# Optimization experiments

Measured on AMD Instinct MI355X. Metric: run time of the kernel, lower is better.

Reference implementation:

```python
import jax, jax.numpy as jnp
import numpy as np

K = 20
BN_EPS = 1e-5


def setup_inputs() -> dict:
    key = jax.random.key(0)
    ks = jax.random.split(key, 6)
    B, N, H = 2, 4096, 384
    s = lambda k, sh, sc: jax.random.normal(k, sh, dtype=jnp.float32) * sc
    return {
        "xyz": jax.random.normal(ks[0], (B, N, 3), dtype=jnp.float32),
        "W1": s(ks[1], (6, 128), 0.2),   "b1": jnp.zeros((128,), jnp.float32),
        "g1": jnp.ones((128,), jnp.float32), "be1": jnp.zeros((128,), jnp.float32),
        "W2": s(ks[2], (128, 256), 0.08), "b2": jnp.zeros((256,), jnp.float32),
        "W3": s(ks[3], (512, 512), 0.05), "b3": jnp.zeros((512,), jnp.float32),
        "g3": jnp.ones((512,), jnp.float32), "be3": jnp.zeros((512,), jnp.float32),
        "W4": s(ks[4], (512, H), 0.05),  "b4": jnp.zeros((H,), jnp.float32),
    }


def _knn_idx(x, k):
    # x: [B,N,3] -> k nearest neighbor indices (incl. self), sorted by distance
    sq = jnp.sum(x * x, axis=-1)                                  # [B,N]
    d2 = sq[:, :, None] + sq[:, None, :] - 2.0 * jnp.einsum('bnd,bmd->bnm', x, x)
    _, idx = jax.lax.top_k(-d2, k)                                # [B,N,k]
    return jax.lax.stop_gradient(idx)


def _bn_relu(h, gamma, beta):
    # BatchNorm1d in training mode: per-channel stats over (batch, length) dims.
    # h: [M, k, C]
    mu = jnp.mean(h, axis=(0, 1), keepdims=True)
    var = jnp.var(h, axis=(0, 1), keepdims=True)  # biased, matches torch BN
    return jax.nn.relu((h - mu) * jax.lax.rsqrt(var + BN_EPS) * gamma + beta)


def reference(xyz, W1, b1, g1, be1, W2, b2, W3, b3, g3, be3, W4, b4):
    B, N, _ = xyz.shape
    idx = _knn_idx(xyz, K)                                        # [B,N,K]
    nbr = jax.vmap(lambda pts, i: pts[i])(xyz, idx)               # [B,N,K,3]
    ctr = xyz[:, :, None, :]
    edge = jnp.concatenate([nbr - ctr, jnp.broadcast_to(ctr, nbr.shape)], axis=-1)
    h = edge.reshape(B * N, K, 6)                                 # [M,K,6]
    # conv1: Conv1d(6,128) -> BN -> ReLU -> Conv1d(128,256)  (kernel-1 convs == matmul)
    h = _bn_relu(h @ W1 + b1, g1, be1)
    h = h @ W2 + b2                                               # [M,K,256]
    gmax = jnp.max(h, axis=1, keepdims=True)                      # [M,1,256]
    f = jnp.concatenate([jnp.broadcast_to(gmax, h.shape), h], axis=-1)  # [M,K,512]
    # conv2: Conv1d(512,512) -> BN -> ReLU -> Conv1d(512,hidden)
    f = _bn_relu(f @ W3 + b3, g3, be3)
    f = f @ W4 + b4                                               # [M,K,H]
    feature = jnp.max(f, axis=1).reshape(B, N, -1)                # [B,N,H]
    return (xyz, feature)
```

## Files before the change

### kernel.cpp

```cpp
#include <hip/hip_runtime.h>
#include <float.h>

#define NPTS_B 4096
#define NPTS 8192
#define KNN 20
#define NSAMP (NPTS*KNN)

typedef __attribute__((ext_vector_type(8))) short bf16x8;
typedef __attribute__((ext_vector_type(4))) float f32x4;

static __device__ __forceinline__ float bf2f(unsigned short u) {
  return __uint_as_float(((unsigned int)u) << 16);
}
static __device__ __forceinline__ unsigned short f2bf(float f) {
  unsigned int u = __float_as_uint(f);
  u += 0x7fffu + ((u >> 16) & 1u);
  return (unsigned short)(u >> 16);
}
static __device__ __forceinline__ void gl_lds16(const void* g, void* l) {
  __builtin_amdgcn_global_load_lds(
      (const __attribute__((address_space(1))) unsigned int*)g,
      (__attribute__((address_space(3))) unsigned int*)l, 16, 0, 0);
}

__global__ __launch_bounds__(256) void wprep_kernel(const float* __restrict__ W3,
                                                    const float* __restrict__ W4,
                                                    const float* __restrict__ W2,
                                                    unsigned short* __restrict__ W3T,
                                                    unsigned short* __restrict__ W4T,
                                                    unsigned short* __restrict__ W2T) {
  int id = blockIdx.x * 256 + threadIdx.x;
  if (id < 512*512) {
    int n = id >> 9, k = id & 511;
    W3T[id] = f2bf(W3[k*512 + n]);
  } else if (id < 512*512 + 384*512) {
    int id2 = id - 512*512;
    int n = id2 >> 9, k = id2 & 511;
    W4T[id2] = f2bf(W4[k*384 + n]);
  } else {
    int id2 = id - (512*512 + 384*512);
    int n = id2 >> 7, k = id2 & 127;
    W2T[id2] = f2bf(W2[k*256 + n]);
  }
}

__global__ __launch_bounds__(256) void xyzprep_kernel(const float* __restrict__ xyz,
                                                      float* __restrict__ xT) {
#pragma clang fp contract(off)
  int j = blockIdx.x * 256 + threadIdx.x;
  int b = j >> 12, jj = j & 4095;
  float x = xyz[j*3+0], y = xyz[j*3+1], z = xyz[j*3+2];
  float sq = (x*x + y*y) + z*z;
  float* base = xT + (size_t)b*16384;
  base[jj] = x; base[4096+jj] = y; base[8192+jj] = z; base[12288+jj] = sq;
}

__global__ __launch_bounds__(256) void knn_kernel(const float* __restrict__ xyz,
                                                  const float* __restrict__ xT,
                                                  int* __restrict__ idx,
                                                  float* __restrict__ out_xyz) {
#pragma clang fp contract(off)
  int p = blockIdx.x;
  int b = p >> 12;
  int base = b << 12;
  int tid = threadIdx.x;
  const float* xb = xT + (size_t)b*16384;
  float xi0 = xyz[p*3+0], xi1 = xyz[p*3+1], xi2 = xyz[p*3+2];
  float sqi = (xi0*xi0 + xi1*xi1) + xi2*xi2;

  __shared__ __align__(16) int hist[4096];
  __shared__ int sL1[256];
  __shared__ int nsel, binB;

#pragma unroll
  for (int u = 0; u < 16; ++u) hist[tid + (u << 8)] = 0;
  if (tid == 0) nsel = 0;
  __syncthreads();

  unsigned long long cand[16];
#pragma unroll
  for (int u = 0; u < 16; ++u) {
    int j = tid + (u << 8);
    float a0 = xb[j], a1 = xb[4096 + j], a2 = xb[8192 + j];
    float sqj = xb[12288 + j];
    float dt  = (xi0*a0 + xi1*a1) + xi2*a2;
    float d2  = (sqi + sqj) - 2.0f*dt;
    unsigned int kb = __float_as_uint(d2);
    cand[u] = ((unsigned long long)kb << 32) | (unsigned int)j;
    atomicAdd(&hist[kb >> 20], 1);
  }
  __syncthreads();

  {
    int s = 0;
#pragma unroll
    for (int u = 0; u < 16; ++u) s += hist[tid*16 + u];
    sL1[tid] = s;
  }
  __syncthreads();

  if (tid < 64) {
    int v = sL1[tid*4] + sL1[tid*4+1] + sL1[tid*4+2] + sL1[tid*4+3];
    int incl = v;
#pragma unroll
    for (int off = 1; off < 64; off <<= 1) {
      int t = __shfl_up(incl, off);
      if (tid >= off) incl += t;
    }
    unsigned long long ball = __ballot(incl >= KNN);
    int L = __ffsll(ball) - 1;
    if (tid == L) {
      int cum = incl - v;
      int bfound = -1;
      for (int t2 = 4*L; t2 < 4*L + 4; ++t2) {
        int s = sL1[t2];
        if (bfound < 0) {
          if (cum + s >= KNN) {
            for (int u = 0; u < 16; ++u) {
              int c = hist[t2*16 + u];
              if (cum + c >= KNN) { bfound = t2*16 + u; break; }
              cum += c;
            }
          } else {
            cum += s;
          }
        }
      }
      binB = bfound;
    }
  }
  __syncthreads();

  int B = binB;
  unsigned long long* list = (unsigned long long*)hist;
#pragma unroll
  for (int u = 0; u < 16; ++u) {
    if ((int)(unsigned int)(cand[u] >> 52) <= B) {
      int pos = atomicAdd(&nsel, 1);
      if (pos < 2048) list[pos] = cand[u];
    }
  }
  __syncthreads();

  int n = nsel; if (n > 2048) n = 2048;
  for (int t = tid; t < n; t += 256) {
    unsigned long long me = list[t];
    int rank = 0;
    for (int i = 0; i < n; ++i) rank += (list[i] < me);
    if (rank < KNN) idx[p*20 + rank] = base + (int)(me & 0xffffffffu);
  }
  if (tid < 3) out_xyz[p*3 + tid] = xyz[p*3 + tid];
}

__global__ __launch_bounds__(256) void h1_moments_kernel(const float* __restrict__ xyz,
                                                         const int* __restrict__ idx,
                                                         float* __restrict__ mbuck) {
  int tid = threadIdx.x, blk = blockIdx.x;
  float A[33] = {};
#pragma unroll
  for (int u = 0; u < 2; ++u) {
    int s = blk*512 + (u << 8) + tid;
    unsigned int p = (unsigned int)s / 20u;
    int jg = idx[s];
    float c0 = xyz[p*3+0], c1 = xyz[p*3+1], c2 = xyz[p*3+2];
    float e[6];
    e[0] = xyz[jg*3+0] - c0; e[1] = xyz[jg*3+1] - c1; e[2] = xyz[jg*3+2] - c2;
    e[3] = c0; e[4] = c1; e[5] = c2;
    int k = 6;
#pragma unroll
    for (int d = 0; d < 6; ++d) {
      A[d] += e[d];
#pragma unroll
      for (int d2 = d; d2 < 6; ++d2) { A[k] = fmaf(e[d], e[d2], A[k]); ++k; }
    }
  }
#pragma unroll
  for (int off = 1; off < 64; off <<= 1) {
#pragma unroll
    for (int i = 0; i < 33; ++i) A[i] += __shfl_xor(A[i], off);
  }
  if ((tid & 63) == 0) {
    int b = ((blk << 2) | (tid >> 6)) & 15;
    for (int i = 0; i < 33; ++i) atomicAdd(&mbuck[b*64 + i], A[i]);
  }
}

__global__ void bn_prep1(const float* __restrict__ W1, const float* __restrict__ b1,
                         const float* __restrict__ g1, const float* __restrict__ be1,
                         const float* __restrict__ mbuck, float* __restrict__ misc) {
  __shared__ float red[33];
  int tid = threadIdx.x;
  if (tid < 33) {
    float s = 0.f;
    for (int b = 0; b < 16; ++b) s += mbuck[b*64 + tid];
    red[tid] = s;
  }
  __syncthreads();
  int c = tid;
  float w[6];
#pragma unroll
  for (int d = 0; d < 6; ++d) w[d] = W1[d*128 + c];
  const float inv = 1.0f / (float)NSAMP;
  float t = 0.f;
#pragma unroll
  for (int d = 0; d < 6; ++d) t = fmaf(w[d], red[d], t);
  t *= inv;
  float Q = 0.f;
  int k = 6;
#pragma unroll
  for (int d = 0; d < 6; ++d) {
#pragma unroll
    for (int d2 = d; d2 < 6; ++d2) {
      float coef = (d == d2) ? w[d]*w[d] : 2.f*w[d]*w[d2];
      Q = fmaf(coef, red[k], Q); ++k;
    }
  }
  Q *= inv;
  float var = Q - t*t;
  float mu = b1[c] + t;
  float a = g1[c] / sqrtf(var + 1e-5f);
  misc[c] = a;
  misc[128 + c] = be1[c] - mu*a;
}

__global__ __launch_bounds__(256) void h2_kernel(const float* __restrict__ xyz,
                                                 const int* __restrict__ idx,
                                                 const float* __restrict__ W1,
                                                 const float* __restrict__ b1,
                                                 const unsigned short* __restrict__ W2T,
                                                 const float* __restrict__ b2,
                                                 const float* __restrict__ misc,
                                                 unsigned short* __restrict__ h2out,
                                                 unsigned short* __restrict__ gmaxout) {
  int p0 = blockIdx.x << 2;
  int tid = threadIdx.x;
  int w = tid >> 6, lane = tid & 63;
  int lr = lane & 15, lg = lane >> 4;
  __shared__ float e[80][6];
  __shared__ __align__(16) unsigned short As[80][136];
  __shared__ float pool[20][264];

  bf16x8 bfr[4][4];
#pragma unroll
  for (int j = 0; j < 4; ++j)
#pragma unroll
    for (int kk = 0; kk < 4; ++kk)
      bfr[j][kk] = *(const bf16x8*)(W2T + (size_t)(w*64 + j*16 + lr)*128 + kk*32 + lg*8);

  if (tid < 80) {
    int pl = (unsigned int)tid / 20u;
    int p = p0 + pl;
    int jg = idx[p0*20 + tid];
    float xi0 = xyz[p*3+0], xi1 = xyz[p*3+1], xi2 = xyz[p*3+2];
    e[tid][0] = xyz[jg*3+0] - xi0;
    e[tid][1] = xyz[jg*3+1] - xi1;
    e[tid][2] = xyz[jg*3+2] - xi2;
    e[tid][3] = xi0; e[tid][4] = xi1; e[tid][5] = xi2;
  }
  __syncthreads();

  {
    int c = tid & 127, half = tid >> 7;
    float w1v[6];
#pragma unroll
    for (int d = 0; d < 6; ++d) w1v[d] = W1[d*128 + c];
    float b1v = b1[c], a1 = misc[c], d1 = misc[128 + c];
#pragma unroll
    for (int u = 0; u < 40; ++u) {
      int row = (u << 1) | half;
      float v = b1v;
#pragma unroll
      for (int d = 0; d < 6; ++d) v = fmaf(e[row][d], w1v[d], v);
      v = fmaxf(fmaf(a1, v, d1), 0.f);
      As[row][c] = f2bf(v);
    }
  }
  __syncthreads();

  f32x4 acc[5][4] = {};
#pragma unroll
  for (int kk = 0; kk < 4; ++kk) {
    bf16x8 a[5];
#pragma unroll
    for (int i = 0; i < 5; ++i)
      a[i] = *(const bf16x8*)&As[i*16 + lr][kk*32 + lg*8];
#pragma unroll
    for (int i = 0; i < 5; ++i)
#pragma unroll
      for (int j = 0; j < 4; ++j)
        acc[i][j] = __builtin_amdgcn_mfma_f32_16x16x32_bf16(a[i], bfr[j][kk], acc[i][j], 0, 0, 0);
  }

  float b2v[4];
#pragma unroll
  for (int j = 0; j < 4; ++j) b2v[j] = b2[w*64 + j*16 + lr];
#pragma unroll
  for (int i = 0; i < 5; ++i) {
    int rbase = p0*20 + i*16 + lg*4;
#pragma unroll
    for (int j = 0; j < 4; ++j) {
      int col = w*64 + j*16 + lr;
      float v0 = acc[i][j][0] + b2v[j];
      float v1 = acc[i][j][1] + b2v[j];
      float v2 = acc[i][j][2] + b2v[j];
      float v3 = acc[i][j][3] + b2v[j];
      h2out[(size_t)(rbase+0)*256 + col] = f2bf(v0);
      h2out[(size_t)(rbase+1)*256 + col] = f2bf(v1);
      h2out[(size_t)(rbase+2)*256 + col] = f2bf(v2);
      h2out[(size_t)(rbase+3)*256 + col] = f2bf(v3);
      pool[i*4 + lg][col] = fmaxf(fmaxf(v0, v1), fmaxf(v2, v3));
    }
  }
  __syncthreads();
#pragma unroll
  for (int l = 0; l < 4; ++l) {
    int id = tid + (l << 8);
    int q = id >> 8, col = id & 255;
    float v = pool[q*5][col];
#pragma unroll
    for (int u = 1; u < 5; ++u) v = fmaxf(v, pool[q*5 + u][col]);
    gmaxout[(size_t)(p0 + q)*256 + col] = f2bf(v);
  }
}

__global__ __launch_bounds__(256) void pgemm_kernel(const unsigned short* __restrict__ gmax,
                                                    const unsigned short* __restrict__ W3T,
                                                    unsigned short* __restrict__ Pg) {
  int bid = blockIdx.x;
  int bm = bid >> 1, bn = bid & 1;
  int m0 = bm << 6, n0 = bn << 8;
  int tid = threadIdx.x;
  int lane = tid & 63, w = tid >> 6;
  int lr = lane & 15, lg = lane >> 4;
  __shared__ __align__(16) char smem[40960];
  unsigned short (*As)[64] = (unsigned short (*)[64])smem;
  unsigned short (*Bs)[64] = (unsigned short (*)[64])(smem + 8192);
  unsigned short (*Cs)[264] = (unsigned short (*)[264])smem;

  int swz = lr >> 1;
  f32x4 acc[4][4] = {};
  for (int kc = 0; kc < 256; kc += 64) {
#pragma unroll
    for (int l = 0; l < 2; ++l) {
      int id = tid + (l << 8);
      int row = id >> 3, ks = id & 7, kg = ks ^ ((id >> 4) & 7);
      gl_lds16(gmax + (size_t)(m0 + row)*256 + kc + (kg << 3), &As[row][ks << 3]);
    }
#pragma unroll
    for (int l = 0; l < 8; ++l) {
      int id = tid + (l << 8);
      int row = id >> 3, ks = id & 7, kg = ks ^ ((id >> 4) & 7);
      gl_lds16(W3T + (size_t)(n0 + row)*512 + kc + (kg << 3), &Bs[row][ks << 3]);
    }
    __syncthreads();
#pragma unroll
    for (int h = 0; h < 2; ++h) {
      int ch = ((h << 2) | lg) ^ swz;
      bf16x8 a[4], b[4];
#pragma unroll
      for (int t = 0; t < 4; ++t)
        a[t] = *(const bf16x8*)&As[t*16 + lr][ch << 3];
#pragma unroll
      for (int t = 0; t < 4; ++t)
        b[t] = *(const bf16x8*)&Bs[w*64 + t*16 + lr][ch << 3];
#pragma unroll
      for (int i = 0; i < 4; ++i)
#pragma unroll
        for (int j = 0; j < 4; ++j)
          acc[i][j] = __builtin_amdgcn_mfma_f32_16x16x32_bf16(a[i], b[j], acc[i][j], 0, 0, 0);
    }
    __syncthreads();
  }
#pragma unroll
  for (int i = 0; i < 4; ++i)
#pragma unroll
    for (int j = 0; j < 4; ++j)
#pragma unroll
      for (int r = 0; r < 4; ++r)
        Cs[i*16 + lg*4 + r][w*64 + j*16 + lr] = f2bf(acc[i][j][r]);
  __syncthreads();
#pragma unroll
  for (int l = 0; l < 8; ++l) {
    int id = tid + (l << 8);
    int row = id >> 5, chk = id & 31;
    *(uint4*)(Pg + (size_t)(m0 + row)*512 + n0 + (chk << 3)) =
        *(const uint4*)&Cs[row][chk << 3];
  }
}

__global__ __launch_bounds__(512, 4) void gemm3_kernel(const unsigned short* __restrict__ h2,
                                                       const unsigned short* __restrict__ Pg,
                                                       const unsigned short* __restrict__ W3T,
                                                       const float* __restrict__ b3,
                                                       unsigned short* __restrict__ h3,
                                                       float* __restrict__ s3buck) {
  int bid = blockIdx.x;
  int grp = bid >> 4, rem = bid & 15;
  int bn = rem >> 3;
  int bm = (grp << 3) | (rem & 7);
  int m0 = bm << 7, n0 = bn << 8;
  int tid = threadIdx.x;
  int lane = tid & 63, w = tid >> 6;
  int mw = w >> 2, nw = w & 3;
  int lr = lane & 15, lg = lane >> 4;
  __shared__ __align__(16) char smem[51200];
  unsigned short (*As)[64] = (unsigned short (*)[64])smem;
  unsigned short (*Bs)[64] = (unsigned short (*)[64])(smem + 16384);
  float* ssum = (float*)(smem + 49152);
  float* ssq  = ssum + 256;
  unsigned short (*Cs)[264] = (unsigned short (*)[264])smem;

  int rS[4], ksS[4], kgS[4];
#pragma unroll
  for (int l = 0; l < 4; ++l) {
    int id = tid + (l << 9);
    rS[l] = id >> 3;
    ksS[l] = id & 7;
    kgS[l] = ksS[l] ^ ((id >> 4) & 7);
  }
  int swz = lr >> 1;

  f32x4 acc[4][4] = {};
  for (int kc = 0; kc < 256; kc += 64) {
#pragma unroll
    for (int l = 0; l < 2; ++l)
      gl_lds16(h2 + (size_t)(m0 + rS[l])*256 + kc + (kgS[l] << 3), &As[rS[l]][ksS[l] << 3]);
#pragma unroll
    for (int l = 0; l < 4; ++l)
      gl_lds16(W3T + (size_t)(n0 + rS[l])*512 + (kc + 256) + (kgS[l] << 3), &Bs[rS[l]][ksS[l] << 3]);
    __syncthreads();
#pragma unroll
    for (int h = 0; h < 2; ++h) {
      int ch = ((h << 2) | lg) ^ swz;
      bf16x8 a[4], b[4];
#pragma unroll
      for (int t = 0; t < 4; ++t)
        a[t] = *(const bf16x8*)&As[mw*64 + t*16 + lr][ch << 3];
#pragma unroll
      for (int t = 0; t < 4; ++t)
        b[t] = *(const bf16x8*)&Bs[nw*64 + t*16 + lr][ch << 3];
#pragma unroll
      for (int i = 0; i < 4; ++i)
#pragma unroll
        for (int j = 0; j < 4; ++j)
          acc[i][j] = __builtin_amdgcn_mfma_f32_16x16x32_bf16(a[i], b[j], acc[i][j], 0, 0, 0);
    }
    __syncthreads();
  }

  if (tid < 256) { ssum[tid] = 0.f; ssq[tid] = 0.f; }
  __syncthreads();
  unsigned int pt[4][4];
#pragma unroll
  for (int i = 0; i < 4; ++i) {
    int rbase = m0 + mw*64 + i*16 + lg*4;
#pragma unroll
    for (int r = 0; r < 4; ++r)
      pt[i][r] = (unsigned int)(rbase + r) / 20u;
  }
#pragma unroll
  for (int half = 0; half < 2; ++half) {
    if (mw == half) {
#pragma unroll
      for (int j = 0; j < 4; ++j) {
        int colL = nw*64 + j*16 + lr;
        float b3v = b3[n0 + colL];
        float sumv = 0.f, sqv = 0.f;
#pragma unroll
        for (int i = 0; i < 4; ++i) {
#pragma unroll
          for (int r = 0; r < 4; ++r) {
            float v = acc[i][j][r] + b3v +
                      bf2f(Pg[(size_t)pt[i][r]*512 + n0 + colL]);
            Cs[i*16 + lg*4 + r][colL] = f2bf(v);
            sumv += v; sqv = fmaf(v, v, sqv);
          }
        }
        sumv += __shfl_xor(sumv, 16); sumv += __shfl_xor(sumv, 32);
        sqv  += __shfl_xor(sqv, 16);  sqv  += __shfl_xor(sqv, 32);
        if (lg == 0) {
          atomicAdd(&ssum[colL], sumv);
          atomicAdd(&ssq[colL], sqv);
        }
      }
    }
    __syncthreads();
#pragma unroll
    for (int l = 0; l < 4; ++l) {
      int id = tid + (l << 9);
      int row = id >> 5, chk = id & 31;
      *(uint4*)(h3 + (size_t)(m0 + half*64 + row)*512 + n0 + (chk << 3)) =
          *(const uint4*)&Cs[row][chk << 3];
    }
    __syncthreads();
  }
  if (tid < 256) {
    int bkt = (bid & 63) * 1024;
    atomicAdd(&s3buck[bkt + n0 + tid], ssum[tid]);
    atomicAdd(&s3buck[bkt + 512 + n0 + tid], ssq[tid]);
  }
}

__global__ void bn_prep3(const float* __restrict__ g3, const float* __restrict__ be3,
                         const float* __restrict__ s3buck, float* __restrict__ misc) {
  int c = threadIdx.x;
  float s = 0.f, q = 0.f;
  for (int b = 0; b < 64; ++b) { s += s3buck[b*1024 + c]; q += s3buck[b*1024 + 512 + c]; }
  const float inv = 1.0f / (float)NSAMP;
  float mu = s * inv;
  float var = q * inv - mu * mu;
  float a = g3[c] / sqrtf(var + 1e-5f);
  misc[256 + c] = a;
  misc[768 + c] = be3[c] - mu * a;
}

__global__ __launch_bounds__(512, 4) void gemm4_kernel(const unsigned short* __restrict__ h3,
                                                       const unsigned short* __restrict__ W4T,
                                                       const float* __restrict__ b4,
                                                       const float* __restrict__ misc,
                                                       float* __restrict__ outf) {
  int bm = blockIdx.x;
  int m0 = bm * 80;
  int tid = threadIdx.x;
  int lane = tid & 63, w = tid >> 6;
  int lr = lane & 15, lg = lane >> 4;
  __shared__ __align__(16) char smem[63488];
  unsigned short (*As)[64] = (unsigned short (*)[64])smem;
  unsigned short (*Bs)[64] = (unsigned short (*)[64])(smem + 10240);
  float (*pool)[392] = (float (*)[392])smem;
  float* af = (float*)(smem + 59392);
  float* df = af + 512;
  if (tid < 512) {
    af[tid] = misc[256 + tid];
    df[tid] = misc[768 + tid];
  }
  __syncthreads();
  f32x4 acc[5][3] = {};

  int arow = tid >> 3, aks = tid & 7, akg = aks ^ ((tid >> 4) & 7);
  uint4 aR0, aR1;
  aR0 = *(const uint4*)(h3 + (size_t)(m0 + arow)*512 + (akg << 3));
  if (tid < 128)
    aR1 = *(const uint4*)(h3 + (size_t)(m0 + 64 + arow)*512 + (akg << 3));

  for (int kc = 0; kc < 512; kc += 64) {
#pragma unroll
    for (int l = 0; l < 6; ++l) {
      int id = tid + (l << 9);
      int row = id >> 3, ks = id & 7, kg = ks ^ ((id >> 4) & 7);
      gl_lds16(W4T + (size_t)row*512 + kc + (kg << 3), &Bs[row][ks << 3]);
    }
    {
      int k0 = kc + (akg << 3);
      unsigned int o[4];
#pragma unroll
      for (int q = 0; q < 4; ++q) {
        unsigned int u = ((const unsigned int*)&aR0)[q];
        float lo = bf2f((unsigned short)(u & 0xffffu));
        float hi = bf2f((unsigned short)(u >> 16));
        lo = fmaxf(fmaf(af[k0 + q*2],     lo, df[k0 + q*2]),     0.f);
        hi = fmaxf(fmaf(af[k0 + q*2 + 1], hi, df[k0 + q*2 + 1]), 0.f);
        o[q] = (unsigned int)f2bf(lo) | ((unsigned int)f2bf(hi) << 16);
      }
      *(uint4*)&As[arow][aks << 3] = *(const uint4*)o;
      if (tid < 128) {
        unsigned int o1[4];
#pragma unroll
        for (int q = 0; q < 4; ++q) {
          unsigned int u = ((const unsigned int*)&aR1)[q];
          float lo = bf2f((unsigned short)(u & 0xffffu));
          float hi = bf2f((unsigned short)(u >> 16));
          lo = fmaxf(fmaf(af[k0 + q*2],     lo, df[k0 + q*2]),     0.f);
          hi = fmaxf(fmaf(af[k0 + q*2 + 1], hi, df[k0 + q*2 + 1]), 0.f);
          o1[q] = (unsigned int)f2bf(lo) | ((unsigned int)f2bf(hi) << 16);
        }
        *(uint4*)&As[64 + arow][aks << 3] = *(const uint4*)o1;
      }
    }
    __syncthreads();
    int kn = kc + 64;
    if (kn < 512) {
      aR0 = *(const uint4*)(h3 + (size_t)(m0 + arow)*512 + kn + (akg << 3));
      if (tid < 128)
        aR1 = *(const uint4*)(h3 + (size_t)(m0 + 64 + arow)*512 + kn + (akg << 3));
    }
#pragma unroll
    for (int h = 0; h < 2; ++h) {
      int ch = ((h << 2) | lg) ^ (lr >> 1);
      bf16x8 a[5], b[3];
#pragma unroll
      for (int t = 0; t < 5; ++t)
        a[t] = *(const bf16x8*)&As[t*16 + lr][ch << 3];
#pragma unroll
      for (int t = 0; t < 3; ++t)
        b[t] = *(const bf16x8*)&Bs[w*48 + t*16 + lr][ch << 3];
#pragma unroll
      for (int i = 0; i < 5; ++i)
#pragma unroll
        for (int j = 0; j < 3; ++j)
          acc[i][j] = __builtin_amdgcn_mfma_f32_16x16x32_bf16(a[i], b[j], acc[i][j], 0, 0, 0);
    }
    __syncthreads();
  }

#pragma unroll
  for (int i = 0; i < 5; ++i)
#pragma unroll
    for (int j = 0; j < 3; ++j) {
      float m = fmaxf(fmaxf(acc[i][j][0], acc[i][j][1]),
                      fmaxf(acc[i][j][2], acc[i][j][3]));
      pool[i*4 + lg][w*48 + j*16 + lr] = m;
    }
  __syncthreads();
#pragma unroll
  for (int l = 0; l < 3; ++l) {
    int id = tid + (l << 9);
    int q = id / 384, c = id - q*384;
    float v = pool[q*5][c];
#pragma unroll
    for (int u = 1; u < 5; ++u) v = fmaxf(v, pool[q*5 + u][c]);
    outf[(size_t)(bm*4 + q)*384 + c] = v + b4[c];
  }
}

extern "C" void kernel_launch(void* const* d_in, const int* in_sizes, int n_in,
                              void* d_out, int out_size, void* d_ws, size_t ws_size,
                              hipStream_t stream) {
  const float* xyz = (const float*)d_in[0];
  const float* W1  = (const float*)d_in[1];
  const float* b1  = (const float*)d_in[2];
  const float* g1  = (const float*)d_in[3];
  const float* be1 = (const float*)d_in[4];
  const float* W2  = (const float*)d_in[5];
  const float* b2  = (const float*)d_in[6];
  const float* W3  = (const float*)d_in[7];
  const float* b3  = (const float*)d_in[8];
  const float* g3  = (const float*)d_in[9];
  const float* be3 = (const float*)d_in[10];
  const float* W4  = (const float*)d_in[11];
  const float* b4  = (const float*)d_in[12];

  char* ws = (char*)d_ws;
  int*            idx    = (int*)ws;
  float*          misc   = (float*)(ws + 0xA0000);
  float*          mbuck  = (float*)(ws + 0xA2000);
  float*          s3buck = (float*)(ws + 0xAA000);
  unsigned short* W3T    = (unsigned short*)(ws + 0xF0000);
  unsigned short* W4T    = (unsigned short*)(ws + 0x170000);
  unsigned short* W2T    = (unsigned short*)(ws + 0x1D0000);
  unsigned short* gmax   = (unsigned short*)(ws + 0x200000);
  unsigned short* h2     = (unsigned short*)(ws + 0x600000);
  unsigned short* h3     = (unsigned short*)(ws + 0x5600000ULL);
  unsigned short* Pg     = (unsigned short*)(ws + 0xF600000ULL);
  float*          xT     = (float*)(ws + 0xFE00000ULL);

  float* ofp   = (float*)d_out;
  float* oxyz  = ofp;
  float* ofeat = ofp + 24576;

  hipMemsetAsync(ws + 0xA2000, 0, 0x48000, stream);

  wprep_kernel<<<(512*512 + 384*512 + 256*128)/256, 256, 0, stream>>>(W3, W4, W2, W3T, W4T, W2T);
  xyzprep_kernel<<<NPTS/256, 256, 0, stream>>>(xyz, xT);
  knn_kernel<<<NPTS, 256, 0, stream>>>(xyz, xT, idx, oxyz);
  h1_moments_kernel<<<NSAMP/512, 256, 0, stream>>>(xyz, idx, mbuck);
  bn_prep1<<<1, 128, 0, stream>>>(W1, b1, g1, be1, mbuck, misc);
  h2_kernel<<<NPTS/4, 256, 0, stream>>>(xyz, idx, W1, b1, W2T, b2, misc, h2, gmax);
  pgemm_kernel<<<256, 256, 0, stream>>>(gmax, W3T, Pg);
  gemm3_kernel<<<(NSAMP/128)*2, 512, 0, stream>>>(h2, Pg, W3T, b3, h3, s3buck);
  bn_prep3<<<1, 512, 0, stream>>>(g3, be3, s3buck, misc);
  gemm4_kernel<<<NPTS/4, 512, 0, stream>>>(h3, W4T, b4, misc, ofeat);
}
```

Baseline: 359.0 us.

## Double-buffer gemm3 LDS tiles with K-step 32 to overlap loads and MFMA

The gemm3 main loop changes from single-buffered 64-wide K chunks to double-buffered 32-wide chunks. The next stage's global-to-LDS loads are issued before computing on the current buffer, and each iteration needs one barrier instead of two. This aims to hide global load latency behind MFMA work. In exchange the loop runs twice as many iterations with fewer MFMAs each, and it uses a new swizzle pattern. Only this one GEMM of the pipeline changes.

```diff
diff --git a/kernel.cpp b/kernel.cpp
--- a/kernel.cpp
+++ b/kernel.cpp
@@ -404,47 +404,49 @@
   int mw = w >> 2, nw = w & 3;
   int lr = lane & 15, lg = lane >> 4;
   __shared__ __align__(16) char smem[51200];
-  unsigned short (*As)[64] = (unsigned short (*)[64])smem;
-  unsigned short (*Bs)[64] = (unsigned short (*)[64])(smem + 16384);
+  unsigned short (*As)[128][32] = (unsigned short (*)[128][32])smem;
+  unsigned short (*Bs)[256][32] = (unsigned short (*)[256][32])(smem + 16384);
   float* ssum = (float*)(smem + 49152);
   float* ssq  = ssum + 256;
   unsigned short (*Cs)[264] = (unsigned short (*)[264])smem;
 
-  int rS[4], ksS[4], kgS[4];
-#pragma unroll
-  for (int l = 0; l < 4; ++l) {
-    int id = tid + (l << 9);
-    rS[l] = id >> 3;
-    ksS[l] = id & 7;
-    kgS[l] = ksS[l] ^ ((id >> 4) & 7);
-  }
-  int swz = lr >> 1;
+  int arow = tid >> 2, aks = tid & 3, akg = aks ^ ((tid >> 3) & 3);
+
+  auto STAGE = [&](int u) {
+    int buf = u & 1;
+    int kc = u << 5;
+    gl_lds16(h2 + (size_t)(m0 + arow)*256 + kc + (akg << 3),
+             &As[buf][arow][aks << 3]);
+#pragma unroll
+    for (int l = 0; l < 2; ++l) {
+      int id = tid + (l << 9);
+      int brow = id >> 2, bks = id & 3, bkg = bks ^ ((id >> 3) & 3);
+      gl_lds16(W3T + (size_t)(n0 + brow)*512 + 256 + kc + (bkg << 3),
+               &Bs[buf][brow][bks << 3]);
+    }
+  };
+
+  int ch = (lg ^ ((lr >> 1) & 3)) << 3;
+
+  STAGE(0);
+  __syncthreads();
 
   f32x4 acc[4][4] = {};
-  for (int kc = 0; kc < 256; kc += 64) {
-#pragma unroll
-    for (int l = 0; l < 2; ++l)
-      gl_lds16(h2 + (size_t)(m0 + rS[l])*256 + kc + (kgS[l] << 3), &As[rS[l]][ksS[l] << 3]);
-#pragma unroll
-    for (int l = 0; l < 4; ++l)
-      gl_lds16(W3T + (size_t)(n0 + rS[l])*512 + (kc + 256) + (kgS[l] << 3), &Bs[rS[l]][ksS[l] << 3]);
-    __syncthreads();
-#pragma unroll
-    for (int h = 0; h < 2; ++h) {
-      int ch = ((h << 2) | lg) ^ swz;
-      bf16x8 a[4], b[4];
-#pragma unroll
-      for (int t = 0; t < 4; ++t)
-        a[t] = *(const bf16x8*)&As[mw*64 + t*16 + lr][ch << 3];
-#pragma unroll
-      for (int t = 0; t < 4; ++t)
-        b[t] = *(const bf16x8*)&Bs[nw*64 + t*16 + lr][ch << 3];
-#pragma unroll
-      for (int i = 0; i < 4; ++i)
-#pragma unroll
-        for (int j = 0; j < 4; ++j)
-          acc[i][j] = __builtin_amdgcn_mfma_f32_16x16x32_bf16(a[i], b[j], acc[i][j], 0, 0, 0);
-    }
+  for (int t = 0; t < 8; ++t) {
+    if (t < 7) STAGE(t + 1);
+    int cur = t & 1;
+    bf16x8 a[4], b[4];
+#pragma unroll
+    for (int i = 0; i < 4; ++i)
+      a[i] = *(const bf16x8*)&As[cur][mw*64 + i*16 + lr][ch];
+#pragma unroll
+    for (int j = 0; j < 4; ++j)
+      b[j] = *(const bf16x8*)&Bs[cur][nw*64 + j*16 + lr][ch];
+#pragma unroll
+    for (int i = 0; i < 4; ++i)
+#pragma unroll
+      for (int j = 0; j < 4; ++j)
+        acc[i][j] = __builtin_amdgcn_mfma_f32_16x16x32_bf16(a[i], b[j], acc[i][j], 0, 0, 0);
     __syncthreads();
   }
 
```

Result: faster. 342.8 us (-4.5%).
